# Optimization experiments

Measured on AMD Instinct MI355X. Metric: run time of the kernel, lower is better.

The kernel has to match this reference:

```python
import jax, jax.numpy as jnp
import numpy as np

N_QUBITS = 6
N_LAYERS = 8
N_CLASSES = 4
BATCH = 262144
DIM = 2 ** N_QUBITS  # 64


def setup_inputs() -> dict:
    key = jax.random.key(0)
    k1, k2, k3, k4 = jax.random.split(key, 4)
    x = jax.random.normal(k1, (BATCH, DIM), dtype=jnp.float32)
    # TorchLayer default init for StronglyEntanglingLayers weights: U(0, 2*pi)
    weights = jax.random.uniform(k2, (N_LAYERS, N_QUBITS, 3), dtype=jnp.float32,
                                 minval=0.0, maxval=2.0 * np.pi)
    fc_w = jax.random.normal(k3, (N_CLASSES, N_QUBITS), dtype=jnp.float32) * 0.3
    fc_b = jax.random.normal(k4, (N_CLASSES,), dtype=jnp.float32) * 0.1
    return {"x": x, "weights": weights, "fc_w": fc_w, "fc_b": fc_b}


def _rot_mats(weights):
    # PennyLane Rot(phi, theta, omega) = RZ(omega) RY(theta) RZ(phi)
    phi, theta, omega = weights[..., 0], weights[..., 1], weights[..., 2]
    c = jnp.cos(theta / 2)
    s = jnp.sin(theta / 2)
    m00 = jnp.exp(-0.5j * (phi + omega)) * c
    m01 = -jnp.exp(0.5j * (phi - omega)) * s
    m10 = jnp.exp(-0.5j * (phi - omega)) * s
    m11 = jnp.exp(0.5j * (phi + omega)) * c
    # [L, n, 2, 2] complex64
    return jnp.stack([jnp.stack([m00, m01], -1), jnp.stack([m10, m11], -1)], -2).astype(jnp.complex64)


def _apply_1q(state, U, q):
    # state: [B, 2, 2, 2, 2, 2, 2]; apply 2x2 gate U on qubit axis q+1
    ax = q + 1
    s = jnp.moveaxis(state, ax, -1)
    s = jnp.einsum('ij,...j->...i', U, s)
    return jnp.moveaxis(s, -1, ax)


def _cnot(state, c, t):
    # flip target qubit t on the control==1 slice of qubit c
    axc = c + 1
    s0 = jax.lax.index_in_dim(state, 0, axis=axc, keepdims=False)
    s1 = jax.lax.index_in_dim(state, 1, axis=axc, keepdims=False)
    t_ax = t + 1 if t < c else t  # target axis after removing control axis
    s1 = jnp.flip(s1, axis=t_ax)
    return jnp.stack([s0, s1], axis=axc)


def _pauli_z_signs():
    # qubit 0 is the most significant bit of the basis-state index
    bits = (jnp.arange(DIM)[:, None] >> jnp.arange(N_QUBITS - 1, -1, -1)[None, :]) & 1
    return (1 - 2 * bits).astype(jnp.float32)  # [DIM, N_QUBITS]


def reference(x, weights, fc_w, fc_b):
    B = x.shape[0]
    # F.normalize(p=2) + AmplitudeEmbedding(normalize=True) -> single L2 normalize
    xn = x / jnp.maximum(jnp.linalg.norm(x, axis=1, keepdims=True), 1e-12)
    state = xn.astype(jnp.complex64).reshape((B,) + (2,) * N_QUBITS)
    U = _rot_mats(weights)  # [L, n, 2, 2]
    for l in range(N_LAYERS):
        for q in range(N_QUBITS):
            state = _apply_1q(state, U[l, q], q)
        r = (l % (N_QUBITS - 1)) + 1  # StronglyEntanglingLayers default ranges
        for q in range(N_QUBITS):
            state = _cnot(state, q, (q + r) % N_QUBITS)
    probs = (state.real ** 2 + state.imag ** 2).reshape(B, DIM)
    expvals = probs @ _pauli_z_signs()  # [B, n] <Z_i>
    return expvals @ fc_w.T + fc_b
```

## Files before the change

### kernel.cpp

```cpp
#include <hip/hip_runtime.h>

#define NQ 6
#define DIM 64
#define NL 8

#define KP  136
#define TPW 8

typedef __attribute__((ext_vector_type(8))) short    short8v;
typedef __attribute__((ext_vector_type(4))) float    floatx4;
typedef __attribute__((ext_vector_type(4))) _Float16 half4v;

__device__ inline short f2bf_rne(float f) {
    unsigned u = __float_as_uint(f);
    u += 0x7FFF + ((u >> 16) & 1);
    return (short)(u >> 16);
}

__global__ __launch_bounds__(64) void qnn_prep(
    const float* __restrict__ wts,
    const float* __restrict__ fc_w,
    void* __restrict__ ws)
{
    __shared__ float gc[48][4];
    const int n   = threadIdx.x;
    const int col = blockIdx.x;

    if (n < 48) {
        float phi = wts[n*3+0], th = wts[n*3+1], om = wts[n*3+2];
        float ch = cosf(0.5f*th), sh = sinf(0.5f*th);
        float p  = 0.5f*(phi+om), m  = 0.5f*(phi-om);
        gc[n][0] = cosf(p)*ch;
        gc[n][1] = sinf(p)*ch;
        gc[n][2] = cosf(m)*sh;
        gc[n][3] = sinf(m)*sh;
    }
    __syncthreads();

    float ar = (n == col) ? 1.0f : 0.0f;
    float ai = 0.0f;

    #pragma unroll
    for (int l = 0; l < NL; ++l) {
        #pragma unroll
        for (int q = 0; q < NQ; ++q) {
            const int g     = l*NQ + q;
            const int shift = 5 - q;
            const int mask  = 1 << shift;
            const int b     = (n >> shift) & 1;
            const float cpch = gc[g][0];
            const float spch = gc[g][1];
            const float cmsh = gc[g][2];
            const float smsh = gc[g][3];
            const float pr = __shfl_xor(ar, mask, 64);
            const float pi = __shfl_xor(ai, mask, 64);
            const float udr = cpch;
            const float udi = b ?  spch : -spch;
            const float uor = b ?  cmsh : -cmsh;
            const float uoi = -smsh;
            const float nr = udr*ar - udi*ai + uor*pr - uoi*pi;
            const float ni = udr*ai + udi*ar + uor*pi + uoi*pr;
            ar = nr; ai = ni;
        }
        const int r = (l % (NQ - 1)) + 1;
        #pragma unroll
        for (int q = 0; q < NQ; ++q) {
            const int t     = (q + r) % NQ;
            const int cmask = 1 << (5 - q);
            const int tmask = 1 << (5 - t);
            const float pr = __shfl_xor(ar, tmask, 64);
            const float pi = __shfl_xor(ai, tmask, 64);
            const bool ctrl = (n & cmask) != 0;
            ar = ctrl ? pr : ar;
            ai = ctrl ? pi : ai;
        }
    }

    unsigned short* Bw = (unsigned short*)ws;
    unsigned short hr = (unsigned short)f2bf_rne(ar);
    float hrf = __uint_as_float((unsigned)hr << 16);
    unsigned short lr = (unsigned short)f2bf_rne(ar - hrf);
    unsigned short hi = (unsigned short)f2bf_rne(ai);
    float hif = __uint_as_float((unsigned)hi << 16);
    unsigned short li = (unsigned short)f2bf_rne(ai - hif);
    Bw[n*KP + col]           = hr;
    Bw[n*KP + 64 + col]      = lr;
    Bw[(64+n)*KP + col]      = hi;
    Bw[(64+n)*KP + 64 + col] = li;

    if (col == 0) {
        const int cp = n & 15;
        const int qd = n >> 4;
        half4v* Mo = (half4v*)((char*)ws + 128*KP*2);
        #pragma unroll
        for (int c2 = 0; c2 < 4; ++c2) {
            half4v h4;
            #pragma unroll
            for (int j = 0; j < 4; ++j) {
                const int i = c2*16 + qd*4 + j;
                float v = 0.f;
                if (cp < 4) {
                    #pragma unroll
                    for (int q = 0; q < NQ; ++q) {
                        const float sgn = 1.0f - 2.0f*(float)((i >> (5-q)) & 1);
                        v = fmaf(sgn, fc_w[cp*NQ + q], v);
                    }
                } else if (cp == 4) {
                    v = 1.0f;
                }
                h4[j] = (_Float16)v;
            }
            Mo[c2*64 + n] = h4;
        }
    }
}

__global__ __launch_bounds__(256, 2) void qnn_main(
    const float* __restrict__ x,
    const float* __restrict__ fc_b,
    const void* __restrict__ wsv,
    float* __restrict__ out)
{
    const int tid  = threadIdx.x;
    const int lane = tid & 63;
    const int w    = tid >> 6;
    const int l15  = lane & 15;
    const int quad = lane >> 4;
    const size_t gw = (size_t)blockIdx.x*4 + w;

    const unsigned short* Wb = (const unsigned short*)wsv;
    short8v wfr[4][8];
    #pragma unroll
    for (int kk = 0; kk < 4; ++kk)
        #pragma unroll
        for (int mt = 0; mt < 8; ++mt)
            wfr[kk][mt] = *(const short8v*)(Wb + (mt*16 + l15)*KP + kk*32 + quad*8);

    const half4v* Mg = (const half4v*)((const char*)wsv + 128*KP*2);
    half4v a2[4];
    #pragma unroll
    for (int c2 = 0; c2 < 4; ++c2) a2[c2] = Mg[c2*64 + lane];

    const float b0 = fc_b[0], b1 = fc_b[1], b2 = fc_b[2], b3 = fc_b[3];

    const float* xbase = x + (gw*TPW*16 + (size_t)l15)*DIM + quad*8;

    float4 xr[2][4];

    xr[0][0] = *(const float4*)(xbase);
    xr[0][1] = *(const float4*)(xbase + 4);
    xr[0][2] = *(const float4*)(xbase + 32);
    xr[0][3] = *(const float4*)(xbase + 36);

#define QNN_COMPUTE(BUF, TI)                                                   \
    {                                                                          \
        short8v xf[2];                                                         \
        _Pragma("unroll")                                                      \
        for (int h = 0; h < 2; ++h) {                                          \
            const float4 u0 = xr[BUF][2*h];                                    \
            const float4 u1 = xr[BUF][2*h + 1];                                \
            short8v a;                                                         \
            a[0]=f2bf_rne(u0.x); a[1]=f2bf_rne(u0.y);                          \
            a[2]=f2bf_rne(u0.z); a[3]=f2bf_rne(u0.w);                          \
            a[4]=f2bf_rne(u1.x); a[5]=f2bf_rne(u1.y);                          \
            a[6]=f2bf_rne(u1.z); a[7]=f2bf_rne(u1.w);                          \
            xf[h] = a;                                                         \
        }                                                                      \
        floatx4 acc[8];                                                        \
        _Pragma("unroll")                                                      \
        for (int mt = 0; mt < 8; ++mt) acc[mt] = (floatx4){0.f,0.f,0.f,0.f};   \
        _Pragma("unroll")                                                      \
        for (int kk = 0; kk < 4; ++kk) {                                       \
            const int h = kk & 1;                                              \
            _Pragma("unroll")                                                  \
            for (int mt = 0; mt < 8; ++mt)                                     \
                acc[mt] = __builtin_amdgcn_mfma_f32_16x16x32_bf16(             \
                    wfr[kk][mt], xf[h], acc[mt], 0, 0, 0);                     \
        }                                                                      \
        floatx4 d2 = (floatx4){0.f,0.f,0.f,0.f};                               \
        _Pragma("unroll")                                                      \
        for (int c2 = 0; c2 < 4; ++c2) {                                       \
            half4v pb;                                                         \
            _Pragma("unroll")                                                  \
            for (int r = 0; r < 4; ++r) {                                      \
                const float re = acc[c2][r];                                   \
                const float im = acc[c2 + 4][r];                               \
                pb[r] = (_Float16)fmaf(re, re, im*im);                         \
            }                                                                  \
            d2 = __builtin_amdgcn_mfma_f32_16x16x16f16(a2[c2], pb, d2, 0,0,0); \
        }                                                                      \
        const float ssv = __shfl_xor(d2[0], 16, 64);                           \
        if (quad == 0) {                                                       \
            const float inv = 1.0f / ssv;                                      \
            float4 o;                                                          \
            o.x = fmaf(d2[0], inv, b0);                                        \
            o.y = fmaf(d2[1], inv, b1);                                        \
            o.z = fmaf(d2[2], inv, b2);                                        \
            o.w = fmaf(d2[3], inv, b3);                                        \
            *(float4*)(out + (gw*TPW + (TI))*16*4 + (size_t)l15*4) = o;        \
        }                                                                      \
    }

    #pragma clang loop unroll(disable)
    for (int t = 0; t < TPW; t += 2) {
        {
            const float* xt = xbase + (size_t)(t + 1) * 1024;
            xr[1][0] = *(const float4*)(xt);
            xr[1][1] = *(const float4*)(xt + 4);
            xr[1][2] = *(const float4*)(xt + 32);
            xr[1][3] = *(const float4*)(xt + 36);
        }
        QNN_COMPUTE(0, t)
        {
            const int tn = (t + 2 < TPW) ? (t + 2) : (TPW - 1);
            const float* xt = xbase + (size_t)tn * 1024;
            xr[0][0] = *(const float4*)(xt);
            xr[0][1] = *(const float4*)(xt + 4);
            xr[0][2] = *(const float4*)(xt + 32);
            xr[0][3] = *(const float4*)(xt + 36);
        }
        QNN_COMPUTE(1, t + 1)
    }
#undef QNN_COMPUTE
}

extern "C" void kernel_launch(void* const* d_in, const int* in_sizes, int n_in,
                              void* d_out, int out_size, void* d_ws, size_t ws_size,
                              hipStream_t stream) {
    const float* x    = (const float*)d_in[0];
    const float* wts  = (const float*)d_in[1];
    const float* fc_w = (const float*)d_in[2];
    const float* fc_b = (const float*)d_in[3];
    float* out = (float*)d_out;

    qnn_prep<<<DIM, DIM, 0, stream>>>(wts, fc_w, d_ws);
    qnn_main<<<512, 256, 0, stream>>>(x, fc_b, d_ws, out);
}
```

Baseline: 110.4 us.

## Switch to fp16 single-term MFMA with LDS-staged coalesced x loads

Replaces the bf16 hi/lo split weight representation (K=128 with 16x16x32 bf16 MFMA) with a single fp16 copy of the unitary (K=64 with 16x16x16 fp16 MFMA). Input rows are now loaded with fully coalesced float4 reads, converted to fp16 and staged through padded LDS, then read back in MFMA fragment layout. Each tile now covers 32 rows, with a fully unrolled double-buffered load/stage/compute sequence. This aims to cut MFMA count and improve global load coalescing, but adds LDS traffic and relies on fp16 precision for the unitary and inputs. There is also no explicit barrier between the LDS stores and reads within a wave.

Result: no change. 108.8 us (-1.5%).

```diff
diff --git a/kernel.cpp b/kernel.cpp
--- a/kernel.cpp
+++ b/kernel.cpp
@@ -4,18 +4,12 @@
 #define DIM 64
 #define NL 8
 
-#define KP  136
-#define TPW 8
-
-typedef __attribute__((ext_vector_type(8))) short    short8v;
+#define WP  72
+#define XP  68
+#define TPW 4
+
 typedef __attribute__((ext_vector_type(4))) float    floatx4;
 typedef __attribute__((ext_vector_type(4))) _Float16 half4v;
-
-__device__ inline short f2bf_rne(float f) {
-    unsigned u = __float_as_uint(f);
-    u += 0x7FFF + ((u >> 16) & 1);
-    return (short)(u >> 16);
-}
 
 __global__ __launch_bounds__(64) void qnn_prep(
     const float* __restrict__ wts,
@@ -76,22 +70,14 @@
         }
     }
 
-    unsigned short* Bw = (unsigned short*)ws;
-    unsigned short hr = (unsigned short)f2bf_rne(ar);
-    float hrf = __uint_as_float((unsigned)hr << 16);
-    unsigned short lr = (unsigned short)f2bf_rne(ar - hrf);
-    unsigned short hi = (unsigned short)f2bf_rne(ai);
-    float hif = __uint_as_float((unsigned)hi << 16);
-    unsigned short li = (unsigned short)f2bf_rne(ai - hif);
-    Bw[n*KP + col]           = hr;
-    Bw[n*KP + 64 + col]      = lr;
-    Bw[(64+n)*KP + col]      = hi;
-    Bw[(64+n)*KP + 64 + col] = li;
+    _Float16* Wf = (_Float16*)ws;
+    Wf[n*WP + col]      = (_Float16)ar;
+    Wf[(64+n)*WP + col] = (_Float16)ai;
 
     if (col == 0) {
         const int cp = n & 15;
         const int qd = n >> 4;
-        half4v* Mo = (half4v*)((char*)ws + 128*KP*2);
+        half4v* Mo = (half4v*)((char*)ws + 128*WP*2);
         #pragma unroll
         for (int c2 = 0; c2 < 4; ++c2) {
             half4v h4;
@@ -121,6 +107,8 @@
     const void* __restrict__ wsv,
     float* __restrict__ out)
 {
+    __shared__ __align__(16) _Float16 Xs[8][32*XP];
+
     const int tid  = threadIdx.x;
     const int lane = tid & 63;
     const int w    = tid >> 6;
@@ -128,99 +116,114 @@
     const int quad = lane >> 4;
     const size_t gw = (size_t)blockIdx.x*4 + w;
 
-    const unsigned short* Wb = (const unsigned short*)wsv;
-    short8v wfr[4][8];
+    const _Float16* Wf = (const _Float16*)wsv;
+    half4v wfr[4][8];
     #pragma unroll
-    for (int kk = 0; kk < 4; ++kk)
+    for (int kc = 0; kc < 4; ++kc)
         #pragma unroll
         for (int mt = 0; mt < 8; ++mt)
-            wfr[kk][mt] = *(const short8v*)(Wb + (mt*16 + l15)*KP + kk*32 + quad*8);
-
-    const half4v* Mg = (const half4v*)((const char*)wsv + 128*KP*2);
+            wfr[kc][mt] = *(const half4v*)(Wf + (mt*16 + l15)*WP + kc*16 + quad*4);
+
+    const half4v* Mg = (const half4v*)((const char*)wsv + 128*WP*2);
     half4v a2[4];
     #pragma unroll
     for (int c2 = 0; c2 < 4; ++c2) a2[c2] = Mg[c2*64 + lane];
 
     const float b0 = fc_b[0], b1 = fc_b[1], b2 = fc_b[2], b3 = fc_b[3];
 
-    const float* xbase = x + (gw*TPW*16 + (size_t)l15)*DIM + quad*8;
-
-    float4 xr[2][4];
-
-    xr[0][0] = *(const float4*)(xbase);
-    xr[0][1] = *(const float4*)(xbase + 4);
-    xr[0][2] = *(const float4*)(xbase + 32);
-    xr[0][3] = *(const float4*)(xbase + 36);
+    const float* xw = x + gw*(TPW*32)*DIM;
+
+#define QNN_LOAD(XRV, TI)                                                      \
+    {                                                                          \
+        const float* xb = xw + (size_t)(TI)*32*DIM;                            \
+        _Pragma("unroll")                                                      \
+        for (int i = 0; i < 8; ++i)                                            \
+            XRV[i] = *(const float4*)(xb + i*256 + lane*4);                    \
+    }
+
+#define QNN_STAGE(XRV, BUF)                                                    \
+    {                                                                          \
+        _Float16* XsR = &Xs[w*2 + (BUF)][0];                                   \
+        _Pragma("unroll")                                                      \
+        for (int i = 0; i < 8; ++i) {                                          \
+            const int ls = 4*i + quad;                                         \
+            half4v h;                                                          \
+            h[0] = (_Float16)XRV[i].x; h[1] = (_Float16)XRV[i].y;              \
+            h[2] = (_Float16)XRV[i].z; h[3] = (_Float16)XRV[i].w;              \
+            *(half4v*)&XsR[ls*XP + 4*l15] = h;                                 \
+        }                                                                      \
+    }
 
 #define QNN_COMPUTE(BUF, TI)                                                   \
     {                                                                          \
-        short8v xf[2];                                                         \
-        _Pragma("unroll")                                                      \
-        for (int h = 0; h < 2; ++h) {                                          \
-            const float4 u0 = xr[BUF][2*h];                                    \
-            const float4 u1 = xr[BUF][2*h + 1];                                \
-            short8v a;                                                         \
-            a[0]=f2bf_rne(u0.x); a[1]=f2bf_rne(u0.y);                          \
-            a[2]=f2bf_rne(u0.z); a[3]=f2bf_rne(u0.w);                          \
-            a[4]=f2bf_rne(u1.x); a[5]=f2bf_rne(u1.y);                          \
-            a[6]=f2bf_rne(u1.z); a[7]=f2bf_rne(u1.w);                          \
-            xf[h] = a;                                                         \
+        const _Float16* XsR = &Xs[w*2 + (BUF)][0];                             \
+        half4v xf[2][4];                                                       \
+        _Pragma("unroll")                                                      \
+        for (int st = 0; st < 2; ++st)                                         \
+            _Pragma("unroll")                                                  \
+            for (int kc = 0; kc < 4; ++kc)                                     \
+                xf[st][kc] = *(const half4v*)                                  \
+                    &XsR[(st*16 + l15)*XP + kc*16 + quad*4];                   \
+        _Pragma("unroll")                                                      \
+        for (int st = 0; st < 2; ++st) {                                       \
+            floatx4 acc[8];                                                    \
+            _Pragma("unroll")                                                  \
+            for (int mt = 0; mt < 8; ++mt)                                     \
+                acc[mt] = (floatx4){0.f, 0.f, 0.f, 0.f};                       \
+            _Pragma("unroll")                                                  \
+            for (int kc = 0; kc < 4; ++kc)                                     \
+                _Pragma("unroll")                                              \
+                for (int mt = 0; mt < 8; ++mt)                                 \
+                    acc[mt] = __builtin_amdgcn_mfma_f32_16x16x16f16(           \
+                        wfr[kc][mt], xf[st][kc], acc[mt], 0, 0, 0);            \
+            floatx4 d2 = (floatx4){0.f, 0.f, 0.f, 0.f};                        \
+            _Pragma("unroll")                                                  \
+            for (int c2 = 0; c2 < 4; ++c2) {                                   \
+                half4v pb;                                                     \
+                _Pragma("unroll")                                              \
+                for (int r = 0; r < 4; ++r) {                                  \
+                    const float re = acc[c2][r];                               \
+                    const float im = acc[c2 + 4][r];                           \
+                    pb[r] = (_Float16)fmaf(re, re, im*im);                     \
+                }                                                              \
+                d2 = __builtin_amdgcn_mfma_f32_16x16x16f16(a2[c2], pb, d2,     \
+                                                           0, 0, 0);           \
+            }                                                                  \
+            const float ssv = __shfl_xor(d2[0], 16, 64);                       \
+            if (quad == 0) {                                                   \
+                const float inv = 1.0f / ssv;                                  \
+                float4 o;                                                      \
+                o.x = fmaf(d2[0], inv, b0);                                    \
+                o.y = fmaf(d2[1], inv, b1);                                    \
+                o.z = fmaf(d2[2], inv, b2);                                    \
+                o.w = fmaf(d2[3], inv, b3);                                    \
+                *(float4*)(out +                                               \
+                    (gw*(TPW*32) + (size_t)(TI)*32 + st*16 + l15)*4) = o;      \
+            }                                                                  \
         }                                                                      \
-        floatx4 acc[8];                                                        \
-        _Pragma("unroll")                                                      \
-        for (int mt = 0; mt < 8; ++mt) acc[mt] = (floatx4){0.f,0.f,0.f,0.f};   \
-        _Pragma("unroll")                                                      \
-        for (int kk = 0; kk < 4; ++kk) {                                       \
-            const int h = kk & 1;                                              \
-            _Pragma("unroll")                                                  \
-            for (int mt = 0; mt < 8; ++mt)                                     \
-                acc[mt] = __builtin_amdgcn_mfma_f32_16x16x32_bf16(             \
-                    wfr[kk][mt], xf[h], acc[mt], 0, 0, 0);                     \
-        }                                                                      \
-        floatx4 d2 = (floatx4){0.f,0.f,0.f,0.f};                               \
-        _Pragma("unroll")                                                      \
-        for (int c2 = 0; c2 < 4; ++c2) {                                       \
-            half4v pb;                                                         \
-            _Pragma("unroll")                                                  \
-            for (int r = 0; r < 4; ++r) {                                      \
-                const float re = acc[c2][r];                                   \
-                const float im = acc[c2 + 4][r];                               \
-                pb[r] = (_Float16)fmaf(re, re, im*im);                         \
-            }                                                                  \
-            d2 = __builtin_amdgcn_mfma_f32_16x16x16f16(a2[c2], pb, d2, 0,0,0); \
-        }                                                                      \
-        const float ssv = __shfl_xor(d2[0], 16, 64);                           \
-        if (quad == 0) {                                                       \
-            const float inv = 1.0f / ssv;                                      \
-            float4 o;                                                          \
-            o.x = fmaf(d2[0], inv, b0);                                        \
-            o.y = fmaf(d2[1], inv, b1);                                        \
-            o.z = fmaf(d2[2], inv, b2);                                        \
-            o.w = fmaf(d2[3], inv, b3);                                        \
-            *(float4*)(out + (gw*TPW + (TI))*16*4 + (size_t)l15*4) = o;        \
-        }                                                                      \
-    }
-
-    #pragma clang loop unroll(disable)
-    for (int t = 0; t < TPW; t += 2) {
-        {
-            const float* xt = xbase + (size_t)(t + 1) * 1024;
-            xr[1][0] = *(const float4*)(xt);
-            xr[1][1] = *(const float4*)(xt + 4);
-            xr[1][2] = *(const float4*)(xt + 32);
-            xr[1][3] = *(const float4*)(xt + 36);
-        }
-        QNN_COMPUTE(0, t)
-        {
-            const int tn = (t + 2 < TPW) ? (t + 2) : (TPW - 1);
-            const float* xt = xbase + (size_t)tn * 1024;
-            xr[0][0] = *(const float4*)(xt);
-            xr[0][1] = *(const float4*)(xt + 4);
-            xr[0][2] = *(const float4*)(xt + 32);
-            xr[0][3] = *(const float4*)(xt + 36);
-        }
-        QNN_COMPUTE(1, t + 1)
-    }
+    }
+
+    float4 xa[8], xb4[8];
+
+    QNN_LOAD(xa, 0)
+    QNN_STAGE(xa, 0)
+
+    QNN_LOAD(xb4, 1)
+    QNN_COMPUTE(0, 0)
+    QNN_STAGE(xb4, 1)
+
+    QNN_LOAD(xa, 2)
+    QNN_COMPUTE(1, 1)
+    QNN_STAGE(xa, 0)
+
+    QNN_LOAD(xb4, 3)
+    QNN_COMPUTE(0, 2)
+    QNN_STAGE(xb4, 1)
+
+    QNN_COMPUTE(1, 3)
+
+#undef QNN_LOAD
+#undef QNN_STAGE
 #undef QNN_COMPUTE
 }
 
```
